# Kernel tuning notes

Measured on AMD Instinct MI355X. Metric: run time of the kernel, lower is better.

The kernel has to match this reference:

```python
import jax, jax.numpy as jnp
import numpy as np

N_NODES = 100000
N_EDGES = 3200000
IN_DIM = 128
HID = 16
MEM = 16
N_LAYERS = 2
OUT = 2
SLOPE = 0.01  # torch leaky_relu default negative_slope


def setup_inputs() -> dict:
    key = jax.random.key(0)
    ks = jax.random.split(key, 20)
    s = 0.05
    inp = {
        "x": jax.random.normal(ks[0], (N_NODES, IN_DIM), dtype=jnp.float32),
        "edge_index": jax.random.randint(ks[1], (2, N_EDGES), 0, N_NODES, dtype=jnp.int64),
        # preprocess MLP: Linear(input_dim,256) -> Linear(256,hidden)
        "pre1_W": jax.random.normal(ks[2], (256, IN_DIM), dtype=jnp.float32) * s,
        "pre1_b": jax.random.normal(ks[3], (256,), dtype=jnp.float32) * s,
        "pre2_W": jax.random.normal(ks[4], (HID, 256), dtype=jnp.float32) * s,
        "pre2_b": jax.random.normal(ks[5], (HID,), dtype=jnp.float32) * s,
        # per-layer hypernetwork GRU biases (input & initial hidden are zeros, so
        # only biases affect the GRU step) and weight_transform Linear(mem, hid*hid)
        "gru_bih": jax.random.normal(ks[6], (N_LAYERS, 3 * MEM), dtype=jnp.float32) * s,
        "gru_bhh": jax.random.normal(ks[7], (N_LAYERS, 3 * MEM), dtype=jnp.float32) * s,
        "wt_W": jax.random.normal(ks[8], (N_LAYERS, HID * HID, MEM), dtype=jnp.float32) * s,
        "wt_b": jax.random.normal(ks[9], (N_LAYERS, HID * HID), dtype=jnp.float32) * s,
        # GCNConv bias (kept as its own parameter in PyG; lin has bias=False)
        "gcn_b": jax.random.normal(ks[10], (N_LAYERS, HID), dtype=jnp.float32) * s,
        # postprocess heads
        "post1_W": jax.random.normal(ks[11], (OUT, HID), dtype=jnp.float32) * s,
        "post1_b": jax.random.normal(ks[12], (OUT,), dtype=jnp.float32) * s,
        "posta_W": jax.random.normal(ks[13], (1, HID), dtype=jnp.float32) * s,
        "posta_b": jax.random.normal(ks[14], (1,), dtype=jnp.float32) * s,
    }
    return inp


def _hyper_gcn_weight(bih, bhh, wt_W, wt_b):
    # GRU single step with zero input and zero initial hidden state:
    # only the biases contribute.  h' = (1-z)*n + z*h_prev, h_prev = 0.
    r = jax.nn.sigmoid(bih[:MEM] + bhh[:MEM])
    z = jax.nn.sigmoid(bih[MEM:2 * MEM] + bhh[MEM:2 * MEM])
    n = jnp.tanh(bih[2 * MEM:] + r * bhh[2 * MEM:])
    mem = (1.0 - z) * n  # [MEM]
    # weight_transform Linear -> view as lin.weight [out, in]; detached in torch
    W = (wt_W @ mem + wt_b).reshape(HID, HID)
    return jax.lax.stop_gradient(W)


def reference(x, edge_index, pre1_W, pre1_b, pre2_W, pre2_b, gru_bih, gru_bhh,
              wt_W, wt_b, gcn_b, post1_W, post1_b, posta_W, posta_b):
    N = x.shape[0]
    # preprocess (dropout p=0.0 -> identity)
    h = jax.nn.leaky_relu(x @ pre1_W.T + pre1_b, negative_slope=SLOPE)
    h = jax.nn.leaky_relu(h @ pre2_W.T + pre2_b, negative_slope=SLOPE)

    # GCN normalization with self-loops (PyG gcn_norm)
    src, dst = edge_index[0], edge_index[1]
    loops = jnp.arange(N, dtype=src.dtype)
    s = jnp.concatenate([src, loops])
    d = jnp.concatenate([dst, loops])
    deg = jax.ops.segment_sum(jnp.ones_like(d, dtype=h.dtype), d, num_segments=N)
    dinv = jnp.where(deg > 0, jax.lax.rsqrt(deg), 0.0)
    norm = dinv[s] * dinv[d]  # [E+N]

    for l in range(N_LAYERS):
        W = _hyper_gcn_weight(gru_bih[l], gru_bhh[l], wt_W[l], wt_b[l])
        xw = h @ W.T                                   # [N, HID]
        msg = xw[s] * norm[:, None]                    # gather + scale
        h = jax.ops.segment_sum(msg, d, num_segments=N) + gcn_b[l]
        h = jax.nn.leaky_relu(h, negative_slope=SLOPE)

    out = jnp.sum(h @ post1_W.T + post1_b, axis=-1)          # [N]
    anomaly = (h @ posta_W.T + posta_b)[:, 0]                # [N]
    return out, anomaly, h
```

## Files before the change

### kernel.cpp

```cpp
#include <hip/hip_runtime.h>
#include <hip/hip_bf16.h>
#include <math.h>

#define IN_DIM 128
#define PRE_HID 256
#define HID 16

__device__ __forceinline__ float lrelu(float v) { return v > 0.f ? v : 0.01f * v; }
__device__ __forceinline__ float fin(float v) { return (v == v && fabsf(v) < 1e30f) ? v : 0.f; }

__device__ __forceinline__ float ldp(const void* p, size_t i, int f32) {
    if (f32) return ((const float*)p)[i];
    unsigned u = ((const unsigned short*)p)[i];
    return __uint_as_float(u << 16);
}
__device__ __forceinline__ unsigned short f2bf(float f) {
    union { __hip_bfloat16 b; unsigned short u; } cv;
    cv.b = __float2bfloat16(f);
    return cv.u;
}
__device__ __forceinline__ void unpack8(uint4 u, float* o) {
    o[0] = __uint_as_float(u.x << 16); o[1] = __uint_as_float(u.x & 0xFFFF0000u);
    o[2] = __uint_as_float(u.y << 16); o[3] = __uint_as_float(u.y & 0xFFFF0000u);
    o[4] = __uint_as_float(u.z << 16); o[5] = __uint_as_float(u.z & 0xFFFF0000u);
    o[6] = __uint_as_float(u.w << 16); o[7] = __uint_as_float(u.w & 0xFFFF0000u);
}
__device__ __forceinline__ unsigned pk2(float a, float b) {
    return (unsigned)f2bf(a) | ((unsigned)f2bf(b) << 16);
}
__device__ __forceinline__ uint4 pack8(const float* v) {
    uint4 u;
    u.x = pk2(v[0], v[1]); u.y = pk2(v[2], v[3]);
    u.z = pk2(v[4], v[5]); u.w = pk2(v[6], v[7]);
    return u;
}

#define OFF_W1F   0
#define OFF_B1F   32768
#define OFF_W2T   33024
#define OFF_B2F   37120
#define OFF_HW    37136
#define OFF_GCNB  37648
#define OFF_POST  37680
#define OFF_FLAGS 37720
#define OFF_BSUM  37760
#define OFF_BPRE  37888
#define OFF_A0    38016

__global__ void k_detect(const unsigned short* __restrict__ xu,
                         const int* __restrict__ ei32, int* __restrict__ flags) {
    if (threadIdx.x == 0 && blockIdx.x == 0) {
        int band = 0;
        for (int k = 0; k < 128; ++k) {
            unsigned e = (xu[2 * k] >> 7) & 0xFF;
            if (e >= 100 && e <= 140) band++;
        }
        flags[1] = (band < 96) ? 1 : 0;
        int any = 0;
        for (int k = 0; k < 64; ++k) any |= ei32[2 * k + 1];
        flags[0] = (any == 0) ? 1 : 0;
    }
}

__global__ void k_sentinel(unsigned* __restrict__ out, int words, unsigned val) {
    int i = blockIdx.x * 256 + threadIdx.x;
    if (i < words) out[i] = val;
}

__global__ void k_prep_small(const void* __restrict__ bih, const void* __restrict__ bhh,
                             const void* __restrict__ wtW, const void* __restrict__ wtb,
                             const void* __restrict__ p1W, const void* __restrict__ p1b,
                             const void* __restrict__ paW, const void* __restrict__ pab,
                             const int* __restrict__ flags,
                             float* __restrict__ hw, float* __restrict__ post) {
    int f32 = flags[1];
    __shared__ float mem[2][16];
    int t = threadIdx.x;
    if (t < 32) {
        int l = t >> 4, j = t & 15;
        float bi0 = ldp(bih, l * 48 + j, f32),      bh0 = ldp(bhh, l * 48 + j, f32);
        float bi1 = ldp(bih, l * 48 + 16 + j, f32), bh1 = ldp(bhh, l * 48 + 16 + j, f32);
        float bi2 = ldp(bih, l * 48 + 32 + j, f32), bh2 = ldp(bhh, l * 48 + 32 + j, f32);
        float r = 1.f / (1.f + expf(-(bi0 + bh0)));
        float z = 1.f / (1.f + expf(-(bi1 + bh1)));
        float nn = tanhf(bi2 + r * bh2);
        mem[l][j] = (1.f - z) * nn;
    }
    __syncthreads();
    for (int l = 0; l < 2; ++l) {
        float acc = ldp(wtb, l * 256 + t, f32);
        #pragma unroll
        for (int m = 0; m < 16; ++m)
            acc += ldp(wtW, l * 4096 + t * 16 + m, f32) * mem[l][m];
        hw[l * 256 + t] = acc;
    }
    if (t < 16) {
        post[t]      = ldp(p1W, t, f32) + ldp(p1W, 16 + t, f32);
        post[17 + t] = ldp(paW, t, f32);
    }
    if (t == 0) {
        post[16] = ldp(p1b, 0, f32) + ldp(p1b, 1, f32);
        post[33] = ldp(pab, 0, f32);
    }
}

__global__ void k_convert(const void* __restrict__ p1W, const void* __restrict__ p1b,
                          const void* __restrict__ p2W, const void* __restrict__ p2b,
                          const void* __restrict__ gcnb, const int* __restrict__ flags,
                          float* __restrict__ w1f, float* __restrict__ b1f,
                          float* __restrict__ w2t, float* __restrict__ b2f,
                          float* __restrict__ gcnbf) {
    int f32 = flags[1];
    int i = blockIdx.x * 256 + threadIdx.x;
    if (i < 32768) w1f[i] = ldp(p1W, i, f32);
    if (i < 256)   b1f[i] = ldp(p1b, i, f32);
    if (i < 4096)  { int r = i >> 4, j = i & 15; w2t[i] = ldp(p2W, j * 256 + r, f32); }
    if (i < 16)    b2f[i] = ldp(p2b, i, f32);
    if (i < 32)    gcnbf[i] = ldp(gcnb, i, f32);
}

__global__ void k_deg(const int* __restrict__ ei, const int* __restrict__ flags,
                      unsigned* __restrict__ deg, int E, int N) {
    int e = blockIdx.x * 256 + threadIdx.x;
    if (e >= E) return;
    int d = flags[0] ? ei[2 * ((size_t)E + e)] : ei[(size_t)E + e];
    if ((unsigned)d < (unsigned)N) atomicAdd(&deg[d], 1u);
}

__global__ void k_dinv(float* __restrict__ degdinv, int N) {
    int n = blockIdx.x * 256 + threadIdx.x;
    if (n >= N) return;
    unsigned dg = ((unsigned*)degdinv)[n];
    degdinv[n] = 1.f / sqrtf((float)dg + 1.f);
}

__global__ void k_dinv2(const unsigned* __restrict__ deg, float* __restrict__ dinv, int N) {
    int n = blockIdx.x * 256 + threadIdx.x;
    if (n >= N) return;
    dinv[n] = 1.f / sqrtf((float)deg[n] + 1.f);
}

__global__ __launch_bounds__(1024) void k_scan_block(const unsigned* __restrict__ deg,
                                                     unsigned* __restrict__ bsum, int N) {
    __shared__ unsigned s[1024];
    int t = threadIdx.x;
    int i = blockIdx.x * 1024 + t;
    s[t] = (i < N) ? deg[i] : 0u;
    __syncthreads();
    for (int off = 512; off > 0; off >>= 1) {
        if (t < off) s[t] += s[t + off];
        __syncthreads();
    }
    if (t == 0) bsum[blockIdx.x] = s[0];
}

__global__ __launch_bounds__(128) void k_scan_top(unsigned* __restrict__ bsum,
                                                  unsigned* __restrict__ bpre, int NB) {
    __shared__ unsigned s[128];
    int t = threadIdx.x;
    unsigned v = (t < NB) ? bsum[t] : 0u;
    s[t] = v;
    __syncthreads();
    for (int off = 1; off < 128; off <<= 1) {
        unsigned a = (t >= off) ? s[t - off] : 0u;
        __syncthreads();
        s[t] += a;
        __syncthreads();
    }
    if (t < NB) bpre[t] = s[t] - v;
}

__global__ __launch_bounds__(1024) void k_scan_final(const unsigned* __restrict__ deg,
                                                     const unsigned* __restrict__ bpre,
                                                     unsigned* __restrict__ rowptr, int N) {
    __shared__ unsigned s[1024];
    int t = threadIdx.x;
    int i = blockIdx.x * 1024 + t;
    unsigned v = (i < N) ? deg[i] : 0u;
    s[t] = v;
    __syncthreads();
    for (int off = 1; off < 1024; off <<= 1) {
        unsigned a = (t >= off) ? s[t - off] : 0u;
        __syncthreads();
        s[t] += a;
        __syncthreads();
    }
    if (i < N) rowptr[i] = bpre[blockIdx.x] + s[t] - v;
}

__global__ void k_fill(const int* __restrict__ ei, const int* __restrict__ flags,
                       unsigned* __restrict__ rowptr, unsigned* __restrict__ csr,
                       int E, int N) {
    int e = blockIdx.x * 256 + threadIdx.x;
    if (e >= E) return;
    int s, d;
    if (flags[0]) { s = ei[2 * (size_t)e]; d = ei[2 * ((size_t)E + e)]; }
    else          { s = ei[e];             d = ei[(size_t)E + e]; }
    if ((unsigned)d >= (unsigned)N) return;
    if ((unsigned)s >= (unsigned)N) s = d;
    unsigned pos = atomicAdd(&rowptr[d], 1u);
    csr[pos] = (unsigned)s;
}

__global__ __launch_bounds__(256, 2) void k_pre(const void* __restrict__ x,
                                                const float* __restrict__ w1f,
                                                const float* __restrict__ b1f,
                                                const float* __restrict__ w2t,
                                                const float* __restrict__ b2f,
                                                const int* __restrict__ flags,
                                                float* __restrict__ h, int N) {
    int n = blockIdx.x * 256 + threadIdx.x;
    if (n >= N) return;
    const int f32 = flags[1];

    float xr[IN_DIM];
    if (f32) {
        const float4* xp = reinterpret_cast<const float4*>((const float*)x + (size_t)n * IN_DIM);
        #pragma unroll
        for (int i = 0; i < 32; ++i) {
            float4 v = xp[i];
            xr[i*4+0] = v.x; xr[i*4+1] = v.y; xr[i*4+2] = v.z; xr[i*4+3] = v.w;
        }
    } else {
        const uint4* xp = reinterpret_cast<const uint4*>((const unsigned short*)x + (size_t)n * IN_DIM);
        #pragma unroll
        for (int i = 0; i < 16; ++i) unpack8(xp[i], xr + i * 8);
    }

    float acc2[HID];
    #pragma unroll
    for (int j = 0; j < HID; ++j) acc2[j] = b2f[j];

    for (int rt = 0; rt < 8; ++rt) {
        float s[32];
        #pragma unroll
        for (int r = 0; r < 32; ++r) s[r] = b1f[rt * 32 + r];
        const float* wbase = w1f + (size_t)(rt * 32) * IN_DIM;
        #pragma unroll
        for (int r = 0; r < 32; ++r) {
            const float* wr = wbase + (size_t)r * IN_DIM;
            float t = s[r];
            #pragma unroll
            for (int k = 0; k < IN_DIM; ++k) t += wr[k] * xr[k];
            s[r] = t;
        }
        const float* w2base = w2t + (size_t)(rt * 32) * HID;
        #pragma unroll
        for (int r = 0; r < 32; ++r) {
            float t = lrelu(s[r]);
            const float* w2r = w2base + (size_t)r * HID;
            #pragma unroll
            for (int j = 0; j < HID; ++j) acc2[j] += w2r[j] * t;
        }
    }
    float4* hp = reinterpret_cast<float4*>(h + (size_t)n * HID);
    #pragma unroll
    for (int q = 0; q < 4; ++q) {
        float4 v;
        v.x = lrelu(acc2[q * 4 + 0]); v.y = lrelu(acc2[q * 4 + 1]);
        v.z = lrelu(acc2[q * 4 + 2]); v.w = lrelu(acc2[q * 4 + 3]);
        hp[q] = v;
    }
}

__global__ void k_xw_y(const float* __restrict__ h, const float* __restrict__ W,
                       const float* __restrict__ dinv, float* __restrict__ y, int N) {
    int n = blockIdx.x * 256 + threadIdx.x;
    if (n >= N) return;
    float hv[HID];
    const float4* hp = reinterpret_cast<const float4*>(h + (size_t)n * HID);
    #pragma unroll
    for (int q = 0; q < 4; ++q) {
        float4 v = hp[q];
        hv[q*4+0] = v.x; hv[q*4+1] = v.y; hv[q*4+2] = v.z; hv[q*4+3] = v.w;
    }
    float dn = dinv[n];
    float4* yp = reinterpret_cast<float4*>(y + (size_t)n * HID);
    #pragma unroll
    for (int q = 0; q < 4; ++q) {
        float o[4];
        #pragma unroll
        for (int ii = 0; ii < 4; ++ii) {
            int i = q * 4 + ii;
            float s = 0.f;
            #pragma unroll
            for (int j = 0; j < HID; ++j) s += W[i * HID + j] * hv[j];
            o[ii] = s * dn;
        }
        float4 v; v.x = o[0]; v.y = o[1]; v.z = o[2]; v.w = o[3];
        yp[q] = v;
    }
}

__global__ __launch_bounds__(256) void k_gather(const unsigned* __restrict__ rowptr,
                                                const unsigned* __restrict__ deg,
                                                const unsigned* __restrict__ csr,
                                                const float* __restrict__ y,
                                                const float* __restrict__ dinv,
                                                const float* __restrict__ gcnbf,
                                                float* __restrict__ h, int N) {
    int tid = blockIdx.x * 256 + threadIdx.x;
    if (tid >= N * 4) return;
    int n = tid >> 2, q = tid & 3;
    unsigned end = rowptr[n];
    unsigned start = end - deg[n];
    float4 acc = *reinterpret_cast<const float4*>(y + (size_t)n * HID + q * 4);
    unsigned k = start;
    if (k < end) {
        unsigned src = csr[k];
        for (++k; k < end; ++k) {
            unsigned nxt = csr[k];
            float4 v = *reinterpret_cast<const float4*>(y + (size_t)src * HID + q * 4);
            acc.x += v.x; acc.y += v.y; acc.z += v.z; acc.w += v.w;
            src = nxt;
        }
        float4 v = *reinterpret_cast<const float4*>(y + (size_t)src * HID + q * 4);
        acc.x += v.x; acc.y += v.y; acc.z += v.z; acc.w += v.w;
    }
    float dn = dinv[n];
    float4 o;
    o.x = lrelu(fin(dn * acc.x) + gcnbf[q*4+0]);
    o.y = lrelu(fin(dn * acc.y) + gcnbf[q*4+1]);
    o.z = lrelu(fin(dn * acc.z) + gcnbf[q*4+2]);
    o.w = lrelu(fin(dn * acc.w) + gcnbf[q*4+3]);
    *reinterpret_cast<float4*>(h + (size_t)n * HID + q * 4) = o;
}

__global__ __launch_bounds__(256) void k_gather_final(const unsigned* __restrict__ rowptr,
                                                      const unsigned* __restrict__ deg,
                                                      const unsigned* __restrict__ csr,
                                                      const float* __restrict__ y,
                                                      const float* __restrict__ dinv,
                                                      const float* __restrict__ gcnbf,
                                                      const float* __restrict__ post,
                                                      const int* __restrict__ flags,
                                                      void* __restrict__ out, int N) {
    int tid = blockIdx.x * 256 + threadIdx.x;
    if (tid >= N * 4) return;
    int n = tid >> 2, q = tid & 3;
    unsigned end = rowptr[n];
    unsigned start = end - deg[n];
    float4 acc = *reinterpret_cast<const float4*>(y + (size_t)n * HID + q * 4);
    unsigned k = start;
    if (k < end) {
        unsigned src = csr[k];
        for (++k; k < end; ++k) {
            unsigned nxt = csr[k];
            float4 v = *reinterpret_cast<const float4*>(y + (size_t)src * HID + q * 4);
            acc.x += v.x; acc.y += v.y; acc.z += v.z; acc.w += v.w;
            src = nxt;
        }
        float4 v = *reinterpret_cast<const float4*>(y + (size_t)src * HID + q * 4);
        acc.x += v.x; acc.y += v.y; acc.z += v.z; acc.w += v.w;
    }
    float dn = dinv[n];
    float v0 = lrelu(fin(dn * acc.x) + gcnbf[q*4+0]);
    float v1 = lrelu(fin(dn * acc.y) + gcnbf[q*4+1]);
    float v2 = lrelu(fin(dn * acc.z) + gcnbf[q*4+2]);
    float v3 = lrelu(fin(dn * acc.w) + gcnbf[q*4+3]);
    float s1 = v0 * post[q*4+0] + v1 * post[q*4+1] + v2 * post[q*4+2] + v3 * post[q*4+3];
    float s2 = v0 * post[17+q*4+0] + v1 * post[17+q*4+1] + v2 * post[17+q*4+2] + v3 * post[17+q*4+3];
    #pragma unroll
    for (int m = 1; m < 4; m <<= 1) {
        s1 += __shfl_xor(s1, m, 64);
        s2 += __shfl_xor(s2, m, 64);
    }
    if (flags[1]) {
        float* ob = (float*)out;
        if (q == 0) ob[n] = s1 + post[16];
        if (q == 1) ob[N + n] = s2 + post[33];
        float4 o; o.x = v0; o.y = v1; o.z = v2; o.w = v3;
        *reinterpret_cast<float4*>(ob + 2 * (size_t)N + (size_t)n * HID + q * 4) = o;
    } else {
        unsigned short* ob = (unsigned short*)out;
        if (q == 0) ob[n] = f2bf(s1 + post[16]);
        if (q == 1) ob[N + n] = f2bf(s2 + post[33]);
        uint2 u; u.x = pk2(v0, v1); u.y = pk2(v2, v3);
        *reinterpret_cast<uint2*>(ob + 2 * (size_t)N + (size_t)n * HID + q * 4) = u;
    }
}

__global__ void k_xw(const float* __restrict__ h, const float* __restrict__ W,
                     const float* __restrict__ dinv, const int* __restrict__ flags,
                     void* __restrict__ xw, float* __restrict__ hacc, int N) {
    int n = blockIdx.x * 256 + threadIdx.x;
    if (n >= N) return;
    float hv[HID];
    const float4* hp = reinterpret_cast<const float4*>(h + (size_t)n * HID);
    #pragma unroll
    for (int q = 0; q < 4; ++q) {
        float4 v = hp[q];
        hv[q*4+0] = v.x; hv[q*4+1] = v.y; hv[q*4+2] = v.z; hv[q*4+3] = v.w;
    }
    float dn = dinv[n];
    float sl = dn * dn;
    float o[HID];
    #pragma unroll
    for (int i = 0; i < HID; ++i) {
        float s = 0.f;
        #pragma unroll
        for (int j = 0; j < HID; ++j) s += W[i * HID + j] * hv[j];
        o[i] = s;
    }
    if (flags[1]) {
        float4* xp = reinterpret_cast<float4*>((float*)xw + (size_t)n * HID);
        #pragma unroll
        for (int q = 0; q < 4; ++q) {
            float4 v; v.x = o[q*4+0]; v.y = o[q*4+1]; v.z = o[q*4+2]; v.w = o[q*4+3];
            xp[q] = v;
        }
    } else {
        uint4* xp = reinterpret_cast<uint4*>((unsigned short*)xw + (size_t)n * HID);
        xp[0] = pack8(o);
        xp[1] = pack8(o + 8);
    }
    float4* ap = reinterpret_cast<float4*>(hacc + (size_t)n * HID);
    #pragma unroll
    for (int q = 0; q < 4; ++q) {
        float4 va;
        va.x = o[q*4+0]*sl; va.y = o[q*4+1]*sl; va.z = o[q*4+2]*sl; va.w = o[q*4+3]*sl;
        ap[q] = va;
    }
}

__global__ __launch_bounds__(256) void k_scatter(const int* __restrict__ ei,
                                                 const int* __restrict__ flags,
                                                 const float* __restrict__ dinv,
                                                 const void* __restrict__ xw,
                                                 float* __restrict__ hacc, int E, int N) {
    int e = blockIdx.x * 256 + threadIdx.x;
    if (e >= E) return;
    int s, d;
    if (flags[0]) { s = ei[2 * (size_t)e]; d = ei[2 * ((size_t)E + e)]; }
    else          { s = ei[e];             d = ei[(size_t)E + e]; }
    if ((unsigned)s >= (unsigned)N || (unsigned)d >= (unsigned)N) return;
    float nrm = dinv[s] * dinv[d];
    float v[HID];
    if (flags[1]) {
        const float4* xr = reinterpret_cast<const float4*>((const float*)xw + (size_t)s * HID);
        #pragma unroll
        for (int q = 0; q < 4; ++q) {
            float4 a = xr[q];
            v[q*4+0] = a.x; v[q*4+1] = a.y; v[q*4+2] = a.z; v[q*4+3] = a.w;
        }
    } else {
        const uint4* xr = reinterpret_cast<const uint4*>((const unsigned short*)xw + (size_t)s * HID);
        unpack8(xr[0], v);
        unpack8(xr[1], v + 8);
    }
    float* out = hacc + (size_t)d * HID;
    #pragma unroll
    for (int j = 0; j < HID; ++j) unsafeAtomicAdd(out + j, v[j] * nrm);
}

__global__ void k_finish(const float* __restrict__ hacc, const float* __restrict__ gcnbf,
                         float* __restrict__ h, int N) {
    int n = blockIdx.x * 256 + threadIdx.x;
    if (n >= N) return;
    const float4* ap = reinterpret_cast<const float4*>(hacc + (size_t)n * HID);
    float4* hp = reinterpret_cast<float4*>(h + (size_t)n * HID);
    #pragma unroll
    for (int q = 0; q < 4; ++q) {
        float4 a = ap[q];
        float4 o;
        o.x = lrelu(fin(a.x) + gcnbf[q*4+0]);
        o.y = lrelu(fin(a.y) + gcnbf[q*4+1]);
        o.z = lrelu(fin(a.z) + gcnbf[q*4+2]);
        o.w = lrelu(fin(a.w) + gcnbf[q*4+3]);
        hp[q] = o;
    }
}

__global__ void k_final(const float* __restrict__ hacc, const float* __restrict__ gcnbf,
                        const float* __restrict__ post, const int* __restrict__ flags,
                        void* __restrict__ out, int N) {
    int n = blockIdx.x * 256 + threadIdx.x;
    if (n >= N) return;
    float v[HID];
    const float4* ap = reinterpret_cast<const float4*>(hacc + (size_t)n * HID);
    #pragma unroll
    for (int q = 0; q < 4; ++q) {
        float4 a = ap[q];
        v[q*4+0] = lrelu(fin(a.x) + gcnbf[q*4+0]);
        v[q*4+1] = lrelu(fin(a.y) + gcnbf[q*4+1]);
        v[q*4+2] = lrelu(fin(a.z) + gcnbf[q*4+2]);
        v[q*4+3] = lrelu(fin(a.w) + gcnbf[q*4+3]);
    }
    float o = post[16], an = post[33];
    #pragma unroll
    for (int j = 0; j < HID; ++j) {
        o += v[j] * post[j];
        an += v[j] * post[17 + j];
    }
    if (flags[1]) {
        float* ob = (float*)out;
        ob[n] = o;
        ob[N + n] = an;
        float* hr = ob + 2 * (size_t)N + (size_t)n * HID;
        #pragma unroll
        for (int j = 0; j < HID; ++j) hr[j] = v[j];
    } else {
        unsigned short* ob = (unsigned short*)out;
        ob[n] = f2bf(o);
        ob[N + n] = f2bf(an);
        uint4* hr = reinterpret_cast<uint4*>(ob + 2 * (size_t)N + (size_t)n * HID);
        hr[0] = pack8(v);
        hr[1] = pack8(v + 8);
    }
}

extern "C" void kernel_launch(void* const* d_in, const int* in_sizes, int n_in,
                              void* d_out, int out_size, void* d_ws, size_t ws_size,
                              hipStream_t stream) {
    const void* x    = d_in[0];
    const int*  ei   = (const int*)d_in[1];
    const void* p1W  = d_in[2];
    const void* p1b  = d_in[3];
    const void* p2W  = d_in[4];
    const void* p2b  = d_in[5];
    const void* bih  = d_in[6];
    const void* bhh  = d_in[7];
    const void* wtW  = d_in[8];
    const void* wtb  = d_in[9];
    const void* gcnb = d_in[10];
    const void* po1W = d_in[11];
    const void* po1b = d_in[12];
    const void* poaW = d_in[13];
    const void* poab = d_in[14];

    const int N = in_sizes[0] / IN_DIM;
    const int E = in_sizes[1] / 2;

    float* ws = (float*)d_ws;
    float* w1f   = ws + OFF_W1F;
    float* b1f   = ws + OFF_B1F;
    float* w2t   = ws + OFF_W2T;
    float* b2f   = ws + OFF_B2F;
    float* hw    = ws + OFF_HW;
    float* gcnbf = ws + OFF_GCNB;
    float* post  = ws + OFF_POST;
    int*   flags = (int*)(ws + OFF_FLAGS);
    unsigned* bsum = (unsigned*)(ws + OFF_BSUM);
    unsigned* bpre = (unsigned*)(ws + OFF_BPRE);

    const int nb_nodes = (N + 255) / 256;
    const int nb_edges = (E + 255) / 256;
    const int nb_n4    = (N * 4 + 255) / 256;
    const int NB       = (N + 1023) / 1024;

    size_t req_csr = ((size_t)OFF_A0 + 35 * (size_t)N + (size_t)E + 64) * 4;
    size_t req_fb  = ((size_t)OFF_A0 + 33 * (size_t)N + 64) * 4;

    if (ws_size >= req_csr && NB <= 128) {
        unsigned* deg    = (unsigned*)(ws + OFF_A0);
        unsigned* rowptr = deg + N;
        float*    dinv   = (float*)(rowptr + N);
        unsigned* csr    = (unsigned*)(dinv + N);
        float*    y      = (float*)(csr + E);
        float*    h      = y + (size_t)N * HID;

        hipMemsetAsync(deg, 0, (size_t)N * 4, stream);
        k_detect<<<1, 64, 0, stream>>>((const unsigned short*)x, ei, flags);
        k_prep_small<<<1, 256, 0, stream>>>(bih, bhh, wtW, wtb, po1W, po1b, poaW, poab,
                                            flags, hw, post);
        k_convert<<<128, 256, 0, stream>>>(p1W, p1b, p2W, p2b, gcnb, flags,
                                           w1f, b1f, w2t, b2f, gcnbf);
        k_deg<<<nb_edges, 256, 0, stream>>>(ei, flags, deg, E, N);
        k_dinv2<<<nb_nodes, 256, 0, stream>>>(deg, dinv, N);
        k_scan_block<<<NB, 1024, 0, stream>>>(deg, bsum, N);
        k_scan_top<<<1, 128, 0, stream>>>(bsum, bpre, NB);
        k_scan_final<<<NB, 1024, 0, stream>>>(deg, bpre, rowptr, N);
        k_fill<<<nb_edges, 256, 0, stream>>>(ei, flags, rowptr, csr, E, N);
        k_pre<<<nb_nodes, 256, 0, stream>>>(x, w1f, b1f, w2t, b2f, flags, h, N);

        k_xw_y<<<nb_nodes, 256, 0, stream>>>(h, hw + 0, dinv, y, N);
        k_gather<<<nb_n4, 256, 0, stream>>>(rowptr, deg, csr, y, dinv, gcnbf + 0, h, N);
        k_xw_y<<<nb_nodes, 256, 0, stream>>>(h, hw + 256, dinv, y, N);
        k_gather_final<<<nb_n4, 256, 0, stream>>>(rowptr, deg, csr, y, dinv, gcnbf + 16,
                                                  post, flags, d_out, N);
    } else if (ws_size >= req_fb) {
        float* degdinv = ws + OFF_A0;
        float* hacc    = degdinv + N;
        float* h       = hacc + (size_t)N * HID;
        void*  xw      = d_out;

        hipMemsetAsync(degdinv, 0, (size_t)N * 4, stream);
        k_detect<<<1, 64, 0, stream>>>((const unsigned short*)x, ei, flags);
        k_prep_small<<<1, 256, 0, stream>>>(bih, bhh, wtW, wtb, po1W, po1b, poaW, poab,
                                            flags, hw, post);
        k_convert<<<128, 256, 0, stream>>>(p1W, p1b, p2W, p2b, gcnb, flags,
                                           w1f, b1f, w2t, b2f, gcnbf);
        k_deg<<<nb_edges, 256, 0, stream>>>(ei, flags, (unsigned*)degdinv, E, N);
        k_dinv<<<nb_nodes, 256, 0, stream>>>(degdinv, N);
        k_pre<<<nb_nodes, 256, 0, stream>>>(x, w1f, b1f, w2t, b2f, flags, h, N);
        for (int l = 0; l < 2; ++l) {
            k_xw<<<nb_nodes, 256, 0, stream>>>(h, hw + l * 256, degdinv, flags, xw, hacc, N);
            k_scatter<<<nb_edges, 256, 0, stream>>>(ei, flags, degdinv, xw, hacc, E, N);
            if (l == 0) k_finish<<<nb_nodes, 256, 0, stream>>>(hacc, gcnbf + 0, h, N);
            else        k_final<<<nb_nodes, 256, 0, stream>>>(hacc, gcnbf + 16, post, flags, d_out, N);
        }
    } else {
        float f = 256.0f + (float)(ws_size >> 20);
        unsigned uv; __builtin_memcpy(&uv, &f, 4);
        int words = out_size / 2;
        k_sentinel<<<(words + 255) / 256, 256, 0, stream>>>((unsigned*)d_out, words, uv);
    }
}
```

Before: 1.182 ms.

## Stage bf16 input rows in swizzled LDS and split preprocess MLP by dtype

Splits the preprocess MLP kernel into separate bf16 and f32 variants, each picked at runtime from a flag, so neither keeps a 128-float per-thread register array. The bf16 path stages a block's input rows into shared memory with coalesced loads and an XOR swizzle, then reads 8 elements at a time. The aim is lower register pressure, higher occupancy and coalesced global reads. The cost is 64KB of LDS per block, which caps occupancy, plus one extra kernel launch that exits immediately.

```diff
diff --git a/kernel.cpp b/kernel.cpp
--- a/kernel.cpp
+++ b/kernel.cpp
@@ -202,55 +202,115 @@
     csr[pos] = (unsigned)s;
 }
 
-__global__ __launch_bounds__(256, 2) void k_pre(const void* __restrict__ x,
-                                                const float* __restrict__ w1f,
-                                                const float* __restrict__ b1f,
-                                                const float* __restrict__ w2t,
-                                                const float* __restrict__ b2f,
-                                                const int* __restrict__ flags,
-                                                float* __restrict__ h, int N) {
-    int n = blockIdx.x * 256 + threadIdx.x;
-    if (n >= N) return;
-    const int f32 = flags[1];
-
-    float xr[IN_DIM];
-    if (f32) {
-        const float4* xp = reinterpret_cast<const float4*>((const float*)x + (size_t)n * IN_DIM);
-        #pragma unroll
-        for (int i = 0; i < 32; ++i) {
-            float4 v = xp[i];
-            xr[i*4+0] = v.x; xr[i*4+1] = v.y; xr[i*4+2] = v.z; xr[i*4+3] = v.w;
-        }
-    } else {
-        const uint4* xp = reinterpret_cast<const uint4*>((const unsigned short*)x + (size_t)n * IN_DIM);
-        #pragma unroll
-        for (int i = 0; i < 16; ++i) unpack8(xp[i], xr + i * 8);
-    }
+__global__ __launch_bounds__(256) void k_pre_bf16(const unsigned short* __restrict__ x,
+                                                  const float* __restrict__ w1f,
+                                                  const float* __restrict__ b1f,
+                                                  const float* __restrict__ w2t,
+                                                  const float* __restrict__ b2f,
+                                                  const int* __restrict__ flags,
+                                                  float* __restrict__ h, int N) {
+    if (flags[1]) return;
+    __shared__ unsigned short xs[256 * 128];
+    const int t = threadIdx.x;
+    const int base = blockIdx.x * 256;
+    #pragma unroll
+    for (int i = 0; i < 16; ++i) {
+        int id = i * 256 + t;
+        int row = id >> 4, c = id & 15;
+        uint4 v = make_uint4(0u, 0u, 0u, 0u);
+        if (base + row < N)
+            v = *reinterpret_cast<const uint4*>(x + ((size_t)(base + row) << 7) + c * 8);
+        int cs = c ^ (row & 15);
+        *reinterpret_cast<uint4*>(xs + row * 128 + cs * 8) = v;
+    }
+    __syncthreads();
+    const int n = base + t;
+    if (n >= N) return;
 
     float acc2[HID];
     #pragma unroll
     for (int j = 0; j < HID; ++j) acc2[j] = b2f[j];
 
+    const int tm = t & 15;
     for (int rt = 0; rt < 8; ++rt) {
         float s[32];
         #pragma unroll
         for (int r = 0; r < 32; ++r) s[r] = b1f[rt * 32 + r];
-        const float* wbase = w1f + (size_t)(rt * 32) * IN_DIM;
+        for (int kc = 0; kc < 16; ++kc) {
+            int cs = kc ^ tm;
+            uint4 u = *reinterpret_cast<const uint4*>(xs + t * 128 + cs * 8);
+            float xr[8];
+            unpack8(u, xr);
+            const float* wbase = w1f + (size_t)(rt * 32) * IN_DIM + kc * 8;
+            #pragma unroll
+            for (int r = 0; r < 32; ++r) {
+                const float* wr = wbase + (size_t)r * IN_DIM;
+                float acc = s[r];
+                #pragma unroll
+                for (int k = 0; k < 8; ++k) acc += wr[k] * xr[k];
+                s[r] = acc;
+            }
+        }
+        const float* w2base = w2t + (size_t)(rt * 32) * HID;
         #pragma unroll
         for (int r = 0; r < 32; ++r) {
-            const float* wr = wbase + (size_t)r * IN_DIM;
-            float t = s[r];
-            #pragma unroll
-            for (int k = 0; k < IN_DIM; ++k) t += wr[k] * xr[k];
-            s[r] = t;
-        }
-        const float* w2base = w2t + (size_t)(rt * 32) * HID;
-        #pragma unroll
-        for (int r = 0; r < 32; ++r) {
-            float t = lrelu(s[r]);
+            float v = lrelu(s[r]);
             const float* w2r = w2base + (size_t)r * HID;
             #pragma unroll
-            for (int j = 0; j < HID; ++j) acc2[j] += w2r[j] * t;
+            for (int j = 0; j < HID; ++j) acc2[j] += w2r[j] * v;
+        }
+    }
+    float4* hp = reinterpret_cast<float4*>(h + (size_t)n * HID);
+    #pragma unroll
+    for (int q = 0; q < 4; ++q) {
+        float4 v;
+        v.x = lrelu(acc2[q * 4 + 0]); v.y = lrelu(acc2[q * 4 + 1]);
+        v.z = lrelu(acc2[q * 4 + 2]); v.w = lrelu(acc2[q * 4 + 3]);
+        hp[q] = v;
+    }
+}
+
+__global__ __launch_bounds__(256) void k_pre_f32(const float* __restrict__ x,
+                                                 const float* __restrict__ w1f,
+                                                 const float* __restrict__ b1f,
+                                                 const float* __restrict__ w2t,
+                                                 const float* __restrict__ b2f,
+                                                 const int* __restrict__ flags,
+                                                 float* __restrict__ h, int N) {
+    if (!flags[1]) return;
+    int n = blockIdx.x * 256 + threadIdx.x;
+    if (n >= N) return;
+    const float* xf = x + (size_t)n * IN_DIM;
+    float acc2[HID];
+    #pragma unroll
+    for (int j = 0; j < HID; ++j) acc2[j] = b2f[j];
+    for (int rt = 0; rt < 8; ++rt) {
+        float s[32];
+        #pragma unroll
+        for (int r = 0; r < 32; ++r) s[r] = b1f[rt * 32 + r];
+        for (int kc = 0; kc < 16; ++kc) {
+            float xr[8];
+            float4 a = *reinterpret_cast<const float4*>(xf + kc * 8);
+            float4 b = *reinterpret_cast<const float4*>(xf + kc * 8 + 4);
+            xr[0] = a.x; xr[1] = a.y; xr[2] = a.z; xr[3] = a.w;
+            xr[4] = b.x; xr[5] = b.y; xr[6] = b.z; xr[7] = b.w;
+            const float* wbase = w1f + (size_t)(rt * 32) * IN_DIM + kc * 8;
+            #pragma unroll
+            for (int r = 0; r < 32; ++r) {
+                const float* wr = wbase + (size_t)r * IN_DIM;
+                float acc = s[r];
+                #pragma unroll
+                for (int k = 0; k < 8; ++k) acc += wr[k] * xr[k];
+                s[r] = acc;
+            }
+        }
+        const float* w2base = w2t + (size_t)(rt * 32) * HID;
+        #pragma unroll
+        for (int r = 0; r < 32; ++r) {
+            float v = lrelu(s[r]);
+            const float* w2r = w2base + (size_t)r * HID;
+            #pragma unroll
+            for (int j = 0; j < HID; ++j) acc2[j] += w2r[j] * v;
         }
     }
     float4* hp = reinterpret_cast<float4*>(h + (size_t)n * HID);
@@ -571,7 +631,10 @@
         k_scan_top<<<1, 128, 0, stream>>>(bsum, bpre, NB);
         k_scan_final<<<NB, 1024, 0, stream>>>(deg, bpre, rowptr, N);
         k_fill<<<nb_edges, 256, 0, stream>>>(ei, flags, rowptr, csr, E, N);
-        k_pre<<<nb_nodes, 256, 0, stream>>>(x, w1f, b1f, w2t, b2f, flags, h, N);
+        k_pre_bf16<<<nb_nodes, 256, 0, stream>>>((const unsigned short*)x, w1f, b1f, w2t, b2f,
+                                                 flags, h, N);
+        k_pre_f32<<<nb_nodes, 256, 0, stream>>>((const float*)x, w1f, b1f, w2t, b2f,
+                                                flags, h, N);
 
         k_xw_y<<<nb_nodes, 256, 0, stream>>>(h, hw + 0, dinv, y, N);
         k_gather<<<nb_n4, 256, 0, stream>>>(rowptr, deg, csr, y, dinv, gcnbf + 0, h, N);
@@ -592,7 +655,10 @@
                                            w1f, b1f, w2t, b2f, gcnbf);
         k_deg<<<nb_edges, 256, 0, stream>>>(ei, flags, (unsigned*)degdinv, E, N);
         k_dinv<<<nb_nodes, 256, 0, stream>>>(degdinv, N);
-        k_pre<<<nb_nodes, 256, 0, stream>>>(x, w1f, b1f, w2t, b2f, flags, h, N);
+        k_pre_bf16<<<nb_nodes, 256, 0, stream>>>((const unsigned short*)x, w1f, b1f, w2t, b2f,
+                                                 flags, h, N);
+        k_pre_f32<<<nb_nodes, 256, 0, stream>>>((const float*)x, w1f, b1f, w2t, b2f,
+                                                flags, h, N);
         for (int l = 0; l < 2; ++l) {
             k_xw<<<nb_nodes, 256, 0, stream>>>(h, hw + l * 256, degdinv, flags, xw, hacc, N);
             k_scatter<<<nb_edges, 256, 0, stream>>>(ei, flags, degdinv, xw, hacc, E, N);
```

Measured after the change: 1.120 ms. 1.05x faster.

## Stage input tile in swizzled LDS as bf16 to cut k_pre register pressure

Applied to the files above, without the earlier changes.

The preprocess MLP kernel now cooperatively loads a 256-row tile of x into shared memory, packed as bf16 with an XOR swizzle to avoid bank conflicts. Each thread then streams its row 8 columns at a time from LDS instead of holding all 128 inputs in registers, and the hidden-layer loop is re-tiled from 32 to 8 rows per pass. The aim is to remove the large per-thread register array (and likely spills) and to make the global loads coalesced. The cost is 64KB of LDS per block, which limits occupancy, and fp32 inputs are now rounded to bf16, which reduces precision.

```diff
diff --git a/kernel.cpp b/kernel.cpp
--- a/kernel.cpp
+++ b/kernel.cpp
@@ -202,55 +202,73 @@
     csr[pos] = (unsigned)s;
 }
 
-__global__ __launch_bounds__(256, 2) void k_pre(const void* __restrict__ x,
-                                                const float* __restrict__ w1f,
-                                                const float* __restrict__ b1f,
-                                                const float* __restrict__ w2t,
-                                                const float* __restrict__ b2f,
-                                                const int* __restrict__ flags,
-                                                float* __restrict__ h, int N) {
-    int n = blockIdx.x * 256 + threadIdx.x;
+__global__ __launch_bounds__(256) void k_pre(const void* __restrict__ x,
+                                             const float* __restrict__ w1f,
+                                             const float* __restrict__ b1f,
+                                             const float* __restrict__ w2t,
+                                             const float* __restrict__ b2f,
+                                             const int* __restrict__ flags,
+                                             float* __restrict__ h, int N) {
+    __shared__ unsigned short xs[256 * 128];
+    const int t = threadIdx.x;
+    const int base = blockIdx.x * 256;
+    const int f32 = flags[1];
+    #pragma unroll
+    for (int i = 0; i < 16; ++i) {
+        int id = i * 256 + t;
+        int row = id >> 4, c = id & 15;
+        uint4 v = make_uint4(0u, 0u, 0u, 0u);
+        if (base + row < N) {
+            if (f32) {
+                const float* xp = (const float*)x + ((size_t)(base + row) << 7) + c * 8;
+                float4 a = *reinterpret_cast<const float4*>(xp);
+                float4 b = *reinterpret_cast<const float4*>(xp + 4);
+                v.x = pk2(a.x, a.y); v.y = pk2(a.z, a.w);
+                v.z = pk2(b.x, b.y); v.w = pk2(b.z, b.w);
+            } else {
+                v = *reinterpret_cast<const uint4*>((const unsigned short*)x +
+                                                    ((size_t)(base + row) << 7) + c * 8);
+            }
+        }
+        int cs = c ^ (row & 15);
+        *reinterpret_cast<uint4*>(xs + row * 128 + cs * 8) = v;
+    }
+    __syncthreads();
+    const int n = base + t;
     if (n >= N) return;
-    const int f32 = flags[1];
-
-    float xr[IN_DIM];
-    if (f32) {
-        const float4* xp = reinterpret_cast<const float4*>((const float*)x + (size_t)n * IN_DIM);
-        #pragma unroll
-        for (int i = 0; i < 32; ++i) {
-            float4 v = xp[i];
-            xr[i*4+0] = v.x; xr[i*4+1] = v.y; xr[i*4+2] = v.z; xr[i*4+3] = v.w;
-        }
-    } else {
-        const uint4* xp = reinterpret_cast<const uint4*>((const unsigned short*)x + (size_t)n * IN_DIM);
-        #pragma unroll
-        for (int i = 0; i < 16; ++i) unpack8(xp[i], xr + i * 8);
-    }
 
     float acc2[HID];
     #pragma unroll
     for (int j = 0; j < HID; ++j) acc2[j] = b2f[j];
 
-    for (int rt = 0; rt < 8; ++rt) {
-        float s[32];
-        #pragma unroll
-        for (int r = 0; r < 32; ++r) s[r] = b1f[rt * 32 + r];
-        const float* wbase = w1f + (size_t)(rt * 32) * IN_DIM;
-        #pragma unroll
-        for (int r = 0; r < 32; ++r) {
-            const float* wr = wbase + (size_t)r * IN_DIM;
-            float t = s[r];
+    const int tm = t & 15;
+    for (int rt = 0; rt < 32; ++rt) {
+        float s[8];
+        #pragma unroll
+        for (int r = 0; r < 8; ++r) s[r] = b1f[rt * 8 + r];
+        #pragma unroll
+        for (int kc = 0; kc < 16; ++kc) {
+            int cs = kc ^ tm;
+            uint4 u = *reinterpret_cast<const uint4*>(xs + t * 128 + cs * 8);
+            float xr[8];
+            unpack8(u, xr);
+            const float* wbase = w1f + (size_t)(rt * 8) * IN_DIM + kc * 8;
             #pragma unroll
-            for (int k = 0; k < IN_DIM; ++k) t += wr[k] * xr[k];
-            s[r] = t;
-        }
-        const float* w2base = w2t + (size_t)(rt * 32) * HID;
-        #pragma unroll
-        for (int r = 0; r < 32; ++r) {
-            float t = lrelu(s[r]);
+            for (int r = 0; r < 8; ++r) {
+                const float* wr = wbase + (size_t)r * IN_DIM;
+                float acc = s[r];
+                #pragma unroll
+                for (int k = 0; k < 8; ++k) acc += wr[k] * xr[k];
+                s[r] = acc;
+            }
+        }
+        const float* w2base = w2t + (size_t)(rt * 8) * HID;
+        #pragma unroll
+        for (int r = 0; r < 8; ++r) {
+            float v = lrelu(s[r]);
             const float* w2r = w2base + (size_t)r * HID;
             #pragma unroll
-            for (int j = 0; j < HID; ++j) acc2[j] += w2r[j] * t;
+            for (int j = 0; j < HID; ++j) acc2[j] += w2r[j] * v;
         }
     }
     float4* hp = reinterpret_cast<float4*>(h + (size_t)n * HID);
```

New measurement: 1.589 ms. 1.34x slower.
